# Kernel optimization log

Hardware: AMD Instinct MI355X
Metric: run time of the kernel (lower is better)

The kernel has to match this reference:

```python
import jax, jax.numpy as jnp
import numpy as np

EPS = 1e-5
B, D_ENT, D_REL = 1024, 400, 400
OUT, KW = 32, 9
N_ENT = 50000


def _bn(x, g, b, axes):
    # batch-norm with batch statistics (training-mode math), eps=1e-5
    mu = jnp.mean(x, axis=axes, keepdims=True)
    var = jnp.var(x, axis=axes, keepdims=True)
    return (x - mu) * jax.lax.rsqrt(var + EPS) * g + b


def setup_inputs() -> dict:
    key = jax.random.key(0)
    ks = jax.random.split(key, 6)
    return {
        "e1_emb": jax.random.normal(ks[0], (B, D_ENT), jnp.float32),
        "rel_emb": jax.random.normal(ks[1], (B, D_REL), jnp.float32),
        "all_ent_w": jax.random.normal(ks[2], (N_ENT, D_ENT), jnp.float32),
        "fc1_w": jax.random.normal(ks[3], (OUT * KW, D_REL), jnp.float32) * 0.05,
        "fc1_b": jnp.zeros((OUT * KW,), jnp.float32),
        "fc_w": jax.random.normal(ks[4], (D_ENT, (D_ENT - KW + 1) * OUT), jnp.float32) * 0.02,
        "fc_b": jnp.zeros((D_ENT,), jnp.float32),
        "bn0_g": jnp.ones((1,), jnp.float32),
        "bn0_b": jnp.zeros((1,), jnp.float32),
        "bn1_g": jnp.ones((OUT,), jnp.float32),
        "bn1_b": jnp.zeros((OUT,), jnp.float32),
        "bn2_g": jnp.ones((D_ENT,), jnp.float32),
        "bn2_b": jnp.zeros((D_ENT,), jnp.float32),
    }


def reference(e1_emb, rel_emb, all_ent_w, fc1_w, fc1_b, fc_w, fc_b,
              bn0_g, bn0_b, bn1_g, bn1_b, bn2_g, bn2_b):
    d = e1_emb.shape[1]
    L = d - KW + 1  # conv output width (kernel_h=1, in_channels=1)

    # bn0: BatchNorm2d(1) over view [B,1,1,d] -> stats over all elements
    x = _bn(e1_emb, bn0_g, bn0_b, axes=(0, 1))  # [B, d]

    # hypernetwork: relation -> per-sample conv kernels [B, OUT, KW]
    k = (rel_emb @ fc1_w.T + fc1_b).reshape(-1, OUT, KW)

    # per-sample 1x9 conv (groups=B) as windows + batched contraction
    # xw[b, l, w] = x[b, l + w]
    xw = jnp.stack([x[:, w:w + L] for w in range(KW)], axis=-1)  # [B, L, KW]
    conv = jnp.einsum('blw,bow->bol', xw, k)  # [B, OUT, L]

    # bn1: BatchNorm2d(OUT), per-channel stats over (batch, width)
    h = _bn(conv, bn1_g[None, :, None], bn1_b[None, :, None], axes=(0, 2))

    # flatten channel-major (matches torch .view(B, -1) on [B, OUT, 1, L])
    h = h.reshape(h.shape[0], OUT * L)
    h = h @ fc_w.T + fc_b  # [B, d]

    # bn2: BatchNorm1d(d), per-feature stats over batch
    h = jax.nn.relu(_bn(h, bn2_g, bn2_b, axes=(0,)))

    return h @ all_ent_w.T  # [B, N_ENT]
```

## Files before the change

kernel.cpp:

```cpp
#include <hip/hip_runtime.h>
#include <stdint.h>

typedef unsigned short u16;
typedef short bf16x8 __attribute__((ext_vector_type(8)));
typedef float f32x4 __attribute__((ext_vector_type(4)));
typedef u16 u16x4 __attribute__((ext_vector_type(4)));
typedef u16 u16x8 __attribute__((ext_vector_type(8)));

#define B_SZ   1024
#define D_IN   400
#define L_OUT  392
#define OC     32
#define KW     9
#define K_FC   12544
#define N_ENT  50000
#define NPAD_ENT 50048
#define KPAD_H 448
#define NPAD_FC 512
#define SPLIT_FC 14

__device__ __forceinline__ u16 f2bf(float f) {
  uint32_t u = __builtin_bit_cast(uint32_t, f);
  u += 0x7FFFu + ((u >> 16) & 1u);
  return (u16)(u >> 16);
}
__device__ __forceinline__ float bf2f(u16 v) {
  uint32_t u = ((uint32_t)v) << 16;
  return __builtin_bit_cast(float, u);
}

__device__ __forceinline__ void gload_lds16(const u16* g, u16* l) {
  __builtin_amdgcn_global_load_lds(
      (const __attribute__((address_space(1))) unsigned int*)g,
      (__attribute__((address_space(3))) unsigned int*)l, 16, 0, 0);
}

__device__ __forceinline__ void block_reduce2(float& s1, float& s2, float* sm) {
  for (int d = 32; d; d >>= 1) { s1 += __shfl_down(s1, d); s2 += __shfl_down(s2, d); }
  int wave = threadIdx.x >> 6, lane = threadIdx.x & 63;
  if (lane == 0) { sm[wave * 2] = s1; sm[wave * 2 + 1] = s2; }
  __syncthreads();
  if (threadIdx.x == 0) {
    s1 = sm[0] + sm[2] + sm[4] + sm[6];
    s2 = sm[1] + sm[3] + sm[5] + sm[7];
  }
}

__global__ __launch_bounds__(256) void red0(const float* __restrict__ e1, float* __restrict__ part0) {
  int t = threadIdx.x;
  int idx = blockIdx.x * 256 + t;
  float s1 = 0.f, s2 = 0.f;
  for (int i = idx; i < B_SZ * D_IN; i += 256 * 256) { float v = e1[i]; s1 += v; s2 += v * v; }
  __shared__ float sm[8];
  block_reduce2(s1, s2, sm);
  if (t == 0) { part0[blockIdx.x * 2] = s1; part0[blockIdx.x * 2 + 1] = s2; }
}

__global__ __launch_bounds__(256) void comb0(const float* __restrict__ part0,
                                             const float* __restrict__ g0,
                                             const float* __restrict__ b0,
                                             float* __restrict__ stats) {
  int t = threadIdx.x;
  float s1 = part0[t * 2], s2 = part0[t * 2 + 1];
  __shared__ float sm[8];
  block_reduce2(s1, s2, sm);
  if (t == 0) {
    const float N = (float)(B_SZ * D_IN);
    float mu = s1 / N, var = s2 / N - mu * mu;
    float a = g0[0] * rsqrtf(var + 1e-5f);
    stats[0] = a;
    stats[1] = b0[0] - mu * a;
  }
}

__global__ __launch_bounds__(256) void fc1_gemm(const float* __restrict__ rel,
                                                const float* __restrict__ W,
                                                const float* __restrict__ bias,
                                                float* __restrict__ outk) {
  __shared__ __align__(16) float As[16 * 68];
  __shared__ __align__(16) float Bs[16 * 68];
  int mt = blockIdx.x, nt = blockIdx.y;
  int t = threadIdx.x;
  int tx = t & 15, ty = t >> 4;
  int lr = t >> 2, lk = (t & 3) * 4;
  float acc[4][4] = {};
  for (int k0 = 0; k0 < 400; k0 += 16) {
    __syncthreads();
    float4 av = *(const float4*)(rel + (size_t)(mt * 64 + lr) * 400 + k0 + lk);
    int brow = nt * 64 + lr;
    float4 bv = {0.f, 0.f, 0.f, 0.f};
    if (brow < 288) bv = *(const float4*)(W + (size_t)brow * 400 + k0 + lk);
    As[(lk + 0) * 68 + lr] = av.x; As[(lk + 1) * 68 + lr] = av.y;
    As[(lk + 2) * 68 + lr] = av.z; As[(lk + 3) * 68 + lr] = av.w;
    Bs[(lk + 0) * 68 + lr] = bv.x; Bs[(lk + 1) * 68 + lr] = bv.y;
    Bs[(lk + 2) * 68 + lr] = bv.z; Bs[(lk + 3) * 68 + lr] = bv.w;
    __syncthreads();
#pragma unroll
    for (int k = 0; k < 16; ++k) {
      float4 a = *(const float4*)(As + k * 68 + ty * 4);
      float4 b = *(const float4*)(Bs + k * 68 + tx * 4);
      float aa[4] = {a.x, a.y, a.z, a.w}, bb[4] = {b.x, b.y, b.z, b.w};
#pragma unroll
      for (int i = 0; i < 4; ++i)
#pragma unroll
        for (int j = 0; j < 4; ++j) acc[i][j] += aa[i] * bb[j];
    }
  }
#pragma unroll
  for (int i = 0; i < 4; ++i) {
    int row = mt * 64 + ty * 4 + i;
#pragma unroll
    for (int j = 0; j < 4; ++j) {
      int col = nt * 64 + tx * 4 + j;
      if (col < 288) outk[(size_t)row * 288 + col] = acc[i][j] + bias[col];
    }
  }
}

__global__ __launch_bounds__(256) void conv_kernel(const float* __restrict__ e1,
                                                   const float* __restrict__ stats,
                                                   const float* __restrict__ kbuf,
                                                   u16* __restrict__ convA,
                                                   float* __restrict__ partial1) {
  int b = blockIdx.x, t = threadIdx.x;
  __shared__ __align__(16) float xs[D_IN];
  __shared__ float ks[OC * KW];
  float a0 = stats[0], b0c = stats[1];
  for (int i = t; i < D_IN; i += 256) xs[i] = e1[(size_t)b * D_IN + i] * a0 + b0c;
  for (int i = t; i < OC * KW; i += 256) ks[i] = kbuf[(size_t)b * (OC * KW) + i];
  __syncthreads();
  int o = t >> 3, sub = t & 7;
  float kw[KW];
#pragma unroll
  for (int w = 0; w < KW; ++w) kw[w] = ks[o * KW + w];
  float s1 = 0.f, s2 = 0.f;
  u16* orow = convA + (size_t)b * K_FC + o * L_OUT;
#pragma unroll
  for (int it = 0; it < 13; ++it) {
    int l = sub * 4 + it * 32;
    if (l < L_OUT) {
      float4 x0 = *(const float4*)(xs + l);
      float4 x1 = *(const float4*)(xs + l + 4);
      float4 x2 = *(const float4*)(xs + l + 8);
      float xv[12] = {x0.x, x0.y, x0.z, x0.w, x1.x, x1.y, x1.z, x1.w, x2.x, x2.y, x2.z, x2.w};
      u16x4 st;
#pragma unroll
      for (int j = 0; j < 4; ++j) {
        float c = 0.f;
#pragma unroll
        for (int w = 0; w < KW; ++w) c += xv[j + w] * kw[w];
        s1 += c; s2 += c * c;
        st[j] = f2bf(c);
      }
      *(u16x4*)(orow + l) = st;
    }
  }
  s1 += __shfl_down(s1, 4); s2 += __shfl_down(s2, 4);
  s1 += __shfl_down(s1, 2); s2 += __shfl_down(s2, 2);
  s1 += __shfl_down(s1, 1); s2 += __shfl_down(s2, 1);
  if (sub == 0) {
    partial1[b * 64 + o] = s1;
    partial1[b * 64 + 32 + o] = s2;
  }
}

__global__ __launch_bounds__(256) void comb1(const float* __restrict__ partial1,
                                             const float* __restrict__ g1,
                                             float* __restrict__ alphaK) {
  __shared__ float red[256];
  __shared__ float ab[32];
  int t = threadIdx.x;
  int s = t & 63, q = t >> 6;
  float acc = 0.f;
  for (int b = q * 256; b < q * 256 + 256; ++b) acc += partial1[b * 64 + s];
  red[t] = acc;
  __syncthreads();
  if (t < 64) red[t] = red[t] + red[t + 64] + red[t + 128] + red[t + 192];
  __syncthreads();
  if (t < 32) {
    const float N = (float)(B_SZ * L_OUT);
    float S1 = red[t], S2 = red[t + 32];
    float mu = S1 / N, var = S2 / N - mu * mu;
    ab[t] = g1[t] * rsqrtf(var + 1e-5f);
  }
  __syncthreads();
  for (int i = t; i < K_FC; i += 256) {
    int o = i / L_OUT;
    alphaK[i] = ab[o];
  }
}

__global__ __launch_bounds__(256) void cvt_fcw(const float* __restrict__ src,
                                               const float* __restrict__ alphaK,
                                               u16* __restrict__ dst) {
  int gid = blockIdx.x * 256 + threadIdx.x;
  int row = gid / 1568, c = gid - row * 1568;
  int k = c * 8;
  u16x8 o = {};
  if (row < 400) {
    float4 f0 = *(const float4*)(src + (size_t)row * K_FC + k);
    float4 f1 = *(const float4*)(src + (size_t)row * K_FC + k + 4);
    float4 a0 = *(const float4*)(alphaK + k);
    float4 a1 = *(const float4*)(alphaK + k + 4);
    o[0] = f2bf(f0.x * a0.x); o[1] = f2bf(f0.y * a0.y);
    o[2] = f2bf(f0.z * a0.z); o[3] = f2bf(f0.w * a0.w);
    o[4] = f2bf(f1.x * a1.x); o[5] = f2bf(f1.y * a1.y);
    o[6] = f2bf(f1.z * a1.z); o[7] = f2bf(f1.w * a1.w);
  }
  *(u16x8*)(dst + (size_t)row * K_FC + k) = o;
}

__global__ __launch_bounds__(256) void cvt_ent(const float* __restrict__ src, u16* __restrict__ dst) {
  int gid = blockIdx.x * 256 + threadIdx.x;
  int row = gid / 56, c = gid - row * 56;
  int k = c * 8;
  u16x8 o = {};
  if (row < N_ENT && k < D_IN) {
    float4 f0 = *(const float4*)(src + (size_t)row * D_IN + k);
    float4 f1 = *(const float4*)(src + (size_t)row * D_IN + k + 4);
    o[0] = f2bf(f0.x); o[1] = f2bf(f0.y); o[2] = f2bf(f0.z); o[3] = f2bf(f0.w);
    o[4] = f2bf(f1.x); o[5] = f2bf(f1.y); o[6] = f2bf(f1.z); o[7] = f2bf(f1.w);
  }
  *(u16x8*)(dst + (size_t)row * KPAD_H + k) = o;
}

__global__ __launch_bounds__(256) void bn2_kernel(const float* __restrict__ part2,
                                                  const float* __restrict__ g2,
                                                  const float* __restrict__ b2,
                                                  u16* __restrict__ hfin) {
  int j0 = blockIdx.x * 16;
  int t = threadIdx.x;
  int tj = t & 15, tb = t >> 4;
  int j = j0 + tj;
  float v[64];
  float s1 = 0.f, s2 = 0.f;
#pragma unroll 2
  for (int i = 0; i < 64; ++i) {
    int b = tb + i * 16;
    float acc = 0.f;
#pragma unroll
    for (int s = 0; s < SPLIT_FC; ++s)
      acc += part2[((size_t)s * B_SZ + b) * NPAD_FC + j];
    v[i] = acc; s1 += acc; s2 += acc * acc;
  }
  __shared__ float sm1[16][17], sm2[16][17];
  sm1[tb][tj] = s1; sm2[tb][tj] = s2;
  __syncthreads();
  __shared__ float albe[2][16];
  if (t < 16) {
    float S1 = 0.f, S2 = 0.f;
#pragma unroll
    for (int r = 0; r < 16; ++r) { S1 += sm1[r][t]; S2 += sm2[r][t]; }
    int jf = j0 + t;
    float al = 0.f, be = 0.f;
    if (jf < D_IN) {
      float mu = S1 / 1024.f, var = S2 / 1024.f - mu * mu;
      al = g2[jf] * rsqrtf(var + 1e-5f);
      be = b2[jf] - mu * al;
    }
    albe[0][t] = al; albe[1][t] = be;
  }
  __syncthreads();
  float al = albe[0][tj], be = albe[1][tj];
#pragma unroll 2
  for (int i = 0; i < 64; ++i) {
    int b = tb + i * 16;
    hfin[(size_t)b * KPAD_H + j] = f2bf(fmaxf(v[i] * al + be, 0.f));
  }
}

__global__ __launch_bounds__(256) void gemm_bt(const u16* __restrict__ A,
                                               const u16* __restrict__ Bm,
                                               float* __restrict__ C,
                                               int Kpad, int mtiles, int ntiles,
                                               int ksteps_total, int ksteps_chunk,
                                               long ldc, int ncols_valid, long csplit_stride,
                                               int xcd_swz) {
  __shared__ __align__(16) u16 As[128 * 64];
  __shared__ __align__(16) u16 Bs[128 * 64];
  int bid = blockIdx.x;
  int mt, nt, sp;
  if (xcd_swz) {
    int r = bid & 7, g = bid >> 3;
    mt = g & 7;
    nt = (g >> 3) * 8 + r;
    sp = 0;
    if (nt >= ntiles) return;
  } else {
    mt = bid % mtiles;
    nt = (bid / mtiles) % ntiles;
    sp = bid / (mtiles * ntiles);
  }
  int kbeg = sp * ksteps_chunk;
  int kend = kbeg + ksteps_chunk;
  if (kend > ksteps_total) kend = ksteps_total;

  int tid = threadIdx.x;
  int wave = tid >> 6, lane = tid & 63;
  int quad = lane >> 4, m16 = lane & 15;
  int rbase = (wave >> 1) * 64, cbase = (wave & 1) * 64;

  const u16* Arow0 = A + (size_t)mt * 128 * Kpad;
  const u16* Brow0 = Bm + (size_t)nt * 128 * Kpad;

  f32x4 acc[4][4] = {};

  for (int kt = kbeg; kt < kend; ++kt) {
    int k0 = kt * 64;
    __syncthreads();
#pragma unroll
    for (int p = 0; p < 4; ++p) {
      int slin = p * 256 + tid;
      int row = slin >> 3;
      int gch = (slin & 7) ^ (row & 7);
      u16* la = As + ((p * 256 + (wave << 6)) << 3);
      u16* lb = Bs + ((p * 256 + (wave << 6)) << 3);
      gload_lds16(Arow0 + (size_t)row * Kpad + k0 + gch * 8, la);
      gload_lds16(Brow0 + (size_t)row * Kpad + k0 + gch * 8, lb);
    }
    __syncthreads();
#pragma unroll
    for (int s = 0; s < 2; ++s) {
      bf16x8 af[4], bfr[4];
#pragma unroll
      for (int i = 0; i < 4; ++i) {
        int ar = rbase + i * 16 + m16;
        af[i] = *(const bf16x8*)(As + ar * 64 + (((s * 4 + quad) ^ (ar & 7)) << 3));
        int bc = cbase + i * 16 + m16;
        bfr[i] = *(const bf16x8*)(Bs + bc * 64 + (((s * 4 + quad) ^ (bc & 7)) << 3));
      }
#pragma unroll
      for (int i = 0; i < 4; ++i)
#pragma unroll
        for (int j = 0; j < 4; ++j)
          acc[i][j] = __builtin_amdgcn_mfma_f32_16x16x32_bf16(af[i], bfr[j], acc[i][j], 0, 0, 0);
    }
  }

  float* Cb = C + (size_t)sp * csplit_stride;
#pragma unroll
  for (int i = 0; i < 4; ++i) {
#pragma unroll
    for (int j = 0; j < 4; ++j) {
      int col = nt * 128 + cbase + j * 16 + m16;
      if (col < ncols_valid) {
        int row0 = mt * 128 + rbase + i * 16 + quad * 4;
#pragma unroll
        for (int r = 0; r < 4; ++r)
          Cb[(size_t)(row0 + r) * ldc + col] = acc[i][j][r];
      }
    }
  }
}

extern "C" void kernel_launch(void* const* d_in, const int* in_sizes, int n_in,
                              void* d_out, int out_size, void* d_ws, size_t ws_size,
                              hipStream_t stream) {
  const float* e1   = (const float*)d_in[0];
  const float* rel  = (const float*)d_in[1];
  const float* entw = (const float*)d_in[2];
  const float* fc1w = (const float*)d_in[3];
  const float* fc1b = (const float*)d_in[4];
  const float* fcw  = (const float*)d_in[5];
  const float* bn0g = (const float*)d_in[7];
  const float* bn0b = (const float*)d_in[8];
  const float* bn1g = (const float*)d_in[9];
  const float* bn2g = (const float*)d_in[11];
  const float* bn2b = (const float*)d_in[12];
  float* out = (float*)d_out;

  char* ws = (char*)d_ws;
  size_t off = 0;
  auto alloc = [&](size_t bytes) -> void* {
    off = (off + 255) & ~(size_t)255;
    void* p = ws + off;
    off += bytes;
    return p;
  };
  float* stats    = (float*)alloc(16 * 4);
  float* part0    = (float*)alloc(512 * 4);
  float* kbuf     = (float*)alloc((size_t)B_SZ * 288 * 4);
  float* partial1 = (float*)alloc((size_t)B_SZ * 64 * 4);
  float* alphaK   = (float*)alloc((size_t)K_FC * 4);
  u16*   convA    = (u16*)alloc((size_t)B_SZ * K_FC * 2);
  u16*   fcwb     = (u16*)alloc((size_t)NPAD_FC * K_FC * 2);
  float* part2    = (float*)alloc((size_t)SPLIT_FC * B_SZ * NPAD_FC * 4);
  u16*   hfin     = (u16*)alloc((size_t)B_SZ * KPAD_H * 2);
  u16*   entb     = (u16*)alloc((size_t)NPAD_ENT * KPAD_H * 2);

  red0<<<256, 256, 0, stream>>>(e1, part0);
  comb0<<<1, 256, 0, stream>>>(part0, bn0g, bn0b, stats);
  fc1_gemm<<<dim3(16, 5), 256, 0, stream>>>(rel, fc1w, fc1b, kbuf);
  conv_kernel<<<B_SZ, 256, 0, stream>>>(e1, stats, kbuf, convA, partial1);
  comb1<<<1, 256, 0, stream>>>(partial1, bn1g, alphaK);
  cvt_fcw<<<3136, 256, 0, stream>>>(fcw, alphaK, fcwb);
  gemm_bt<<<8 * 4 * SPLIT_FC, 256, 0, stream>>>(convA, fcwb, part2, K_FC, 8, 4, 196, 14,
                                                (long)NPAD_FC, NPAD_FC, (long)B_SZ * NPAD_FC, 0);
  bn2_kernel<<<KPAD_H / 16, 256, 0, stream>>>(part2, bn2g, bn2b, hfin);
  cvt_ent<<<10948, 256, 0, stream>>>(entw, entb);
  gemm_bt<<<8 * 392, 256, 0, stream>>>(hfin, entb, out, KPAD_H, 8, 391, 7, 7,
                                       (long)N_ENT, N_ENT, 0, 1);
}
```

Measured before the change: 555.4 us.

## Fuse fp32-to-bf16 weight conversion into GEMM loads and parallelize bn2

Drops the separate cvt_fcw and cvt_ent passes. Both GEMMs now read the fp32 weights directly, scaling and converting them to bf16 in registers before writing to LDS, which removes a full write and re-read of the converted weight buffers. The single-pass bn2 kernel, which ran on only 28 blocks, is split into stats, combine and apply kernels spread over 448 blocks. In exchange, the B-operand loads become synchronous register loads instead of async global-to-LDS loads. Each entity tile's weights are also converted again by all 8 M-tiles, which repeats conversion ALU work and doubles fp32 reads per tile.

After: 587.0 us. +5.7%, slower.

```diff
diff --git a/kernel.cpp b/kernel.cpp
--- a/kernel.cpp
+++ b/kernel.cpp
@@ -14,7 +14,6 @@
 #define KW     9
 #define K_FC   12544
 #define N_ENT  50000
-#define NPAD_ENT 50048
 #define KPAD_H 448
 #define NPAD_FC 512
 #define SPLIT_FC 14
@@ -23,10 +22,6 @@
   uint32_t u = __builtin_bit_cast(uint32_t, f);
   u += 0x7FFFu + ((u >> 16) & 1u);
   return (u16)(u >> 16);
-}
-__device__ __forceinline__ float bf2f(u16 v) {
-  uint32_t u = ((uint32_t)v) << 16;
-  return __builtin_bit_cast(float, u);
 }
 
 __device__ __forceinline__ void gload_lds16(const u16* g, u16* l) {
@@ -190,118 +185,22 @@
   }
 }
 
-__global__ __launch_bounds__(256) void cvt_fcw(const float* __restrict__ src,
+__global__ __launch_bounds__(256) void gemm_fc(const u16* __restrict__ A,
+                                               const float* __restrict__ Bw,
                                                const float* __restrict__ alphaK,
-                                               u16* __restrict__ dst) {
-  int gid = blockIdx.x * 256 + threadIdx.x;
-  int row = gid / 1568, c = gid - row * 1568;
-  int k = c * 8;
-  u16x8 o = {};
-  if (row < 400) {
-    float4 f0 = *(const float4*)(src + (size_t)row * K_FC + k);
-    float4 f1 = *(const float4*)(src + (size_t)row * K_FC + k + 4);
-    float4 a0 = *(const float4*)(alphaK + k);
-    float4 a1 = *(const float4*)(alphaK + k + 4);
-    o[0] = f2bf(f0.x * a0.x); o[1] = f2bf(f0.y * a0.y);
-    o[2] = f2bf(f0.z * a0.z); o[3] = f2bf(f0.w * a0.w);
-    o[4] = f2bf(f1.x * a1.x); o[5] = f2bf(f1.y * a1.y);
-    o[6] = f2bf(f1.z * a1.z); o[7] = f2bf(f1.w * a1.w);
-  }
-  *(u16x8*)(dst + (size_t)row * K_FC + k) = o;
-}
-
-__global__ __launch_bounds__(256) void cvt_ent(const float* __restrict__ src, u16* __restrict__ dst) {
-  int gid = blockIdx.x * 256 + threadIdx.x;
-  int row = gid / 56, c = gid - row * 56;
-  int k = c * 8;
-  u16x8 o = {};
-  if (row < N_ENT && k < D_IN) {
-    float4 f0 = *(const float4*)(src + (size_t)row * D_IN + k);
-    float4 f1 = *(const float4*)(src + (size_t)row * D_IN + k + 4);
-    o[0] = f2bf(f0.x); o[1] = f2bf(f0.y); o[2] = f2bf(f0.z); o[3] = f2bf(f0.w);
-    o[4] = f2bf(f1.x); o[5] = f2bf(f1.y); o[6] = f2bf(f1.z); o[7] = f2bf(f1.w);
-  }
-  *(u16x8*)(dst + (size_t)row * KPAD_H + k) = o;
-}
-
-__global__ __launch_bounds__(256) void bn2_kernel(const float* __restrict__ part2,
-                                                  const float* __restrict__ g2,
-                                                  const float* __restrict__ b2,
-                                                  u16* __restrict__ hfin) {
-  int j0 = blockIdx.x * 16;
-  int t = threadIdx.x;
-  int tj = t & 15, tb = t >> 4;
-  int j = j0 + tj;
-  float v[64];
-  float s1 = 0.f, s2 = 0.f;
-#pragma unroll 2
-  for (int i = 0; i < 64; ++i) {
-    int b = tb + i * 16;
-    float acc = 0.f;
-#pragma unroll
-    for (int s = 0; s < SPLIT_FC; ++s)
-      acc += part2[((size_t)s * B_SZ + b) * NPAD_FC + j];
-    v[i] = acc; s1 += acc; s2 += acc * acc;
-  }
-  __shared__ float sm1[16][17], sm2[16][17];
-  sm1[tb][tj] = s1; sm2[tb][tj] = s2;
-  __syncthreads();
-  __shared__ float albe[2][16];
-  if (t < 16) {
-    float S1 = 0.f, S2 = 0.f;
-#pragma unroll
-    for (int r = 0; r < 16; ++r) { S1 += sm1[r][t]; S2 += sm2[r][t]; }
-    int jf = j0 + t;
-    float al = 0.f, be = 0.f;
-    if (jf < D_IN) {
-      float mu = S1 / 1024.f, var = S2 / 1024.f - mu * mu;
-      al = g2[jf] * rsqrtf(var + 1e-5f);
-      be = b2[jf] - mu * al;
-    }
-    albe[0][t] = al; albe[1][t] = be;
-  }
-  __syncthreads();
-  float al = albe[0][tj], be = albe[1][tj];
-#pragma unroll 2
-  for (int i = 0; i < 64; ++i) {
-    int b = tb + i * 16;
-    hfin[(size_t)b * KPAD_H + j] = f2bf(fmaxf(v[i] * al + be, 0.f));
-  }
-}
-
-__global__ __launch_bounds__(256) void gemm_bt(const u16* __restrict__ A,
-                                               const u16* __restrict__ Bm,
-                                               float* __restrict__ C,
-                                               int Kpad, int mtiles, int ntiles,
-                                               int ksteps_total, int ksteps_chunk,
-                                               long ldc, int ncols_valid, long csplit_stride,
-                                               int xcd_swz) {
+                                               float* __restrict__ C) {
   __shared__ __align__(16) u16 As[128 * 64];
   __shared__ __align__(16) u16 Bs[128 * 64];
   int bid = blockIdx.x;
-  int mt, nt, sp;
-  if (xcd_swz) {
-    int r = bid & 7, g = bid >> 3;
-    mt = g & 7;
-    nt = (g >> 3) * 8 + r;
-    sp = 0;
-    if (nt >= ntiles) return;
-  } else {
-    mt = bid % mtiles;
-    nt = (bid / mtiles) % ntiles;
-    sp = bid / (mtiles * ntiles);
-  }
-  int kbeg = sp * ksteps_chunk;
-  int kend = kbeg + ksteps_chunk;
-  if (kend > ksteps_total) kend = ksteps_total;
+  int mt = bid & 7, nt = (bid >> 3) & 3, sp = bid >> 5;
+  int kbeg = sp * (196 / SPLIT_FC), kend = kbeg + (196 / SPLIT_FC);
 
   int tid = threadIdx.x;
   int wave = tid >> 6, lane = tid & 63;
   int quad = lane >> 4, m16 = lane & 15;
   int rbase = (wave >> 1) * 64, cbase = (wave & 1) * 64;
 
-  const u16* Arow0 = A + (size_t)mt * 128 * Kpad;
-  const u16* Brow0 = Bm + (size_t)nt * 128 * Kpad;
+  const u16* Arow0 = A + (size_t)mt * 128 * K_FC;
 
   f32x4 acc[4][4] = {};
 
@@ -313,10 +212,28 @@
       int slin = p * 256 + tid;
       int row = slin >> 3;
       int gch = (slin & 7) ^ (row & 7);
-      u16* la = As + ((p * 256 + (wave << 6)) << 3);
-      u16* lb = Bs + ((p * 256 + (wave << 6)) << 3);
-      gload_lds16(Arow0 + (size_t)row * Kpad + k0 + gch * 8, la);
-      gload_lds16(Brow0 + (size_t)row * Kpad + k0 + gch * 8, lb);
+      gload_lds16(Arow0 + (size_t)row * K_FC + k0 + gch * 8,
+                  As + ((p * 256 + (wave << 6)) << 3));
+    }
+#pragma unroll
+    for (int p = 0; p < 4; ++p) {
+      int slin = p * 256 + tid;
+      int row = slin >> 3;
+      int gch = (slin & 7) ^ (row & 7);
+      int gr = nt * 128 + row;
+      int k = k0 + gch * 8;
+      u16x8 bv = {};
+      if (gr < D_IN) {
+        float4 f0 = *(const float4*)(Bw + (size_t)gr * K_FC + k);
+        float4 f1 = *(const float4*)(Bw + (size_t)gr * K_FC + k + 4);
+        float4 a0 = *(const float4*)(alphaK + k);
+        float4 a1 = *(const float4*)(alphaK + k + 4);
+        bv[0] = f2bf(f0.x * a0.x); bv[1] = f2bf(f0.y * a0.y);
+        bv[2] = f2bf(f0.z * a0.z); bv[3] = f2bf(f0.w * a0.w);
+        bv[4] = f2bf(f1.x * a1.x); bv[5] = f2bf(f1.y * a1.y);
+        bv[6] = f2bf(f1.z * a1.z); bv[7] = f2bf(f1.w * a1.w);
+      }
+      *(u16x8*)(Bs + ((size_t)slin << 3)) = bv;
     }
     __syncthreads();
 #pragma unroll
@@ -337,17 +254,165 @@
     }
   }
 
-  float* Cb = C + (size_t)sp * csplit_stride;
+  float* Cb = C + (size_t)sp * B_SZ * NPAD_FC;
 #pragma unroll
   for (int i = 0; i < 4; ++i) {
 #pragma unroll
     for (int j = 0; j < 4; ++j) {
       int col = nt * 128 + cbase + j * 16 + m16;
-      if (col < ncols_valid) {
+      int row0 = mt * 128 + rbase + i * 16 + quad * 4;
+#pragma unroll
+      for (int r = 0; r < 4; ++r)
+        Cb[(size_t)(row0 + r) * NPAD_FC + col] = acc[i][j][r];
+    }
+  }
+}
+
+__global__ __launch_bounds__(256) void bn2_stats(const float* __restrict__ part2,
+                                                 float* __restrict__ pstat) {
+  int jg = blockIdx.x % 28, bc = blockIdx.x / 28;
+  int t = threadIdx.x;
+  int tj = t & 15, tb = t >> 4;
+  int j = jg * 16 + tj;
+  float s1 = 0.f, s2 = 0.f;
+#pragma unroll
+  for (int i = 0; i < 4; ++i) {
+    int b = bc * 64 + tb + i * 16;
+    float acc = 0.f;
+#pragma unroll
+    for (int s = 0; s < SPLIT_FC; ++s)
+      acc += part2[((size_t)s * B_SZ + b) * NPAD_FC + j];
+    s1 += acc; s2 += acc * acc;
+  }
+  __shared__ float sm1[16][17], sm2[16][17];
+  sm1[tb][tj] = s1; sm2[tb][tj] = s2;
+  __syncthreads();
+  if (t < 16) {
+    float S1 = 0.f, S2 = 0.f;
+#pragma unroll
+    for (int r = 0; r < 16; ++r) { S1 += sm1[r][t]; S2 += sm2[r][t]; }
+    pstat[blockIdx.x * 32 + t] = S1;
+    pstat[blockIdx.x * 32 + 16 + t] = S2;
+  }
+}
+
+__global__ __launch_bounds__(448) void bn2_comb(const float* __restrict__ pstat,
+                                                const float* __restrict__ g2,
+                                                const float* __restrict__ b2,
+                                                float* __restrict__ albe) {
+  int j = threadIdx.x;
+  int jg = j >> 4, tj = j & 15;
+  float S1 = 0.f, S2 = 0.f;
+#pragma unroll
+  for (int bc = 0; bc < 16; ++bc) {
+    S1 += pstat[(jg + 28 * bc) * 32 + tj];
+    S2 += pstat[(jg + 28 * bc) * 32 + 16 + tj];
+  }
+  float al = 0.f, be = 0.f;
+  if (j < D_IN) {
+    float mu = S1 / 1024.f, var = S2 / 1024.f - mu * mu;
+    al = g2[j] * rsqrtf(var + 1e-5f);
+    be = b2[j] - mu * al;
+  }
+  albe[j] = al;
+  albe[KPAD_H + j] = be;
+}
+
+__global__ __launch_bounds__(256) void bn2_apply(const float* __restrict__ part2,
+                                                 const float* __restrict__ albe,
+                                                 u16* __restrict__ hfin) {
+  int jg = blockIdx.x % 28, bc = blockIdx.x / 28;
+  int t = threadIdx.x;
+  int tj = t & 15, tb = t >> 4;
+  int j = jg * 16 + tj;
+  float al = albe[j], be = albe[KPAD_H + j];
+#pragma unroll
+  for (int i = 0; i < 4; ++i) {
+    int b = bc * 64 + tb + i * 16;
+    float acc = 0.f;
+#pragma unroll
+    for (int s = 0; s < SPLIT_FC; ++s)
+      acc += part2[((size_t)s * B_SZ + b) * NPAD_FC + j];
+    hfin[(size_t)b * KPAD_H + j] = f2bf(fmaxf(acc * al + be, 0.f));
+  }
+}
+
+__global__ __launch_bounds__(256) void gemm_ent(const u16* __restrict__ A,
+                                                const float* __restrict__ Bw,
+                                                float* __restrict__ C) {
+  __shared__ __align__(16) u16 As[128 * 64];
+  __shared__ __align__(16) u16 Bs[128 * 64];
+  int bid = blockIdx.x;
+  int r = bid & 7, g = bid >> 3;
+  int mt = g & 7;
+  int nt = (g >> 3) * 8 + r;
+  if (nt >= 391) return;
+
+  int tid = threadIdx.x;
+  int wave = tid >> 6, lane = tid & 63;
+  int quad = lane >> 4, m16 = lane & 15;
+  int rbase = (wave >> 1) * 64, cbase = (wave & 1) * 64;
+
+  const u16* Arow0 = A + (size_t)mt * 128 * KPAD_H;
+
+  f32x4 acc[4][4] = {};
+
+  for (int kt = 0; kt < 7; ++kt) {
+    int k0 = kt * 64;
+    __syncthreads();
+#pragma unroll
+    for (int p = 0; p < 4; ++p) {
+      int slin = p * 256 + tid;
+      int row = slin >> 3;
+      int gch = (slin & 7) ^ (row & 7);
+      gload_lds16(Arow0 + (size_t)row * KPAD_H + k0 + gch * 8,
+                  As + ((p * 256 + (wave << 6)) << 3));
+    }
+#pragma unroll
+    for (int p = 0; p < 4; ++p) {
+      int slin = p * 256 + tid;
+      int row = slin >> 3;
+      int gch = (slin & 7) ^ (row & 7);
+      int gr = nt * 128 + row;
+      int k = k0 + gch * 8;
+      u16x8 bv = {};
+      if (gr < N_ENT && k < D_IN) {
+        float4 f0 = *(const float4*)(Bw + (size_t)gr * D_IN + k);
+        float4 f1 = *(const float4*)(Bw + (size_t)gr * D_IN + k + 4);
+        bv[0] = f2bf(f0.x); bv[1] = f2bf(f0.y); bv[2] = f2bf(f0.z); bv[3] = f2bf(f0.w);
+        bv[4] = f2bf(f1.x); bv[5] = f2bf(f1.y); bv[6] = f2bf(f1.z); bv[7] = f2bf(f1.w);
+      }
+      *(u16x8*)(Bs + ((size_t)slin << 3)) = bv;
+    }
+    __syncthreads();
+#pragma unroll
+    for (int s = 0; s < 2; ++s) {
+      bf16x8 af[4], bfr[4];
+#pragma unroll
+      for (int i = 0; i < 4; ++i) {
+        int ar = rbase + i * 16 + m16;
+        af[i] = *(const bf16x8*)(As + ar * 64 + (((s * 4 + quad) ^ (ar & 7)) << 3));
+        int bc = cbase + i * 16 + m16;
+        bfr[i] = *(const bf16x8*)(Bs + bc * 64 + (((s * 4 + quad) ^ (bc & 7)) << 3));
+      }
+#pragma unroll
+      for (int i = 0; i < 4; ++i)
+#pragma unroll
+        for (int j = 0; j < 4; ++j)
+          acc[i][j] = __builtin_amdgcn_mfma_f32_16x16x32_bf16(af[i], bfr[j], acc[i][j], 0, 0, 0);
+    }
+  }
+
+#pragma unroll
+  for (int i = 0; i < 4; ++i) {
+#pragma unroll
+    for (int j = 0; j < 4; ++j) {
+      int col = nt * 128 + cbase + j * 16 + m16;
+      if (col < N_ENT) {
         int row0 = mt * 128 + rbase + i * 16 + quad * 4;
 #pragma unroll
-        for (int r = 0; r < 4; ++r)
-          Cb[(size_t)(row0 + r) * ldc + col] = acc[i][j][r];
+        for (int r2 = 0; r2 < 4; ++r2)
+          C[(size_t)(row0 + r2) * N_ENT + col] = acc[i][j][r2];
       }
     }
   }
@@ -383,21 +448,19 @@
   float* partial1 = (float*)alloc((size_t)B_SZ * 64 * 4);
   float* alphaK   = (float*)alloc((size_t)K_FC * 4);
   u16*   convA    = (u16*)alloc((size_t)B_SZ * K_FC * 2);
-  u16*   fcwb     = (u16*)alloc((size_t)NPAD_FC * K_FC * 2);
   float* part2    = (float*)alloc((size_t)SPLIT_FC * B_SZ * NPAD_FC * 4);
+  float* pstat    = (float*)alloc((size_t)448 * 32 * 4);
+  float* albe     = (float*)alloc((size_t)2 * KPAD_H * 4);
   u16*   hfin     = (u16*)alloc((size_t)B_SZ * KPAD_H * 2);
-  u16*   entb     = (u16*)alloc((size_t)NPAD_ENT * KPAD_H * 2);
 
   red0<<<256, 256, 0, stream>>>(e1, part0);
   comb0<<<1, 256, 0, stream>>>(part0, bn0g, bn0b, stats);
   fc1_gemm<<<dim3(16, 5), 256, 0, stream>>>(rel, fc1w, fc1b, kbuf);
   conv_kernel<<<B_SZ, 256, 0, stream>>>(e1, stats, kbuf, convA, partial1);
   comb1<<<1, 256, 0, stream>>>(partial1, bn1g, alphaK);
-  cvt_fcw<<<3136, 256, 0, stream>>>(fcw, alphaK, fcwb);
-  gemm_bt<<<8 * 4 * SPLIT_FC, 256, 0, stream>>>(convA, fcwb, part2, K_FC, 8, 4, 196, 14,
-                                                (long)NPAD_FC, NPAD_FC, (long)B_SZ * NPAD_FC, 0);
-  bn2_kernel<<<KPAD_H / 16, 256, 0, stream>>>(part2, bn2g, bn2b, hfin);
-  cvt_ent<<<10948, 256, 0, stream>>>(entw, entb);
-  gemm_bt<<<8 * 392, 256, 0, stream>>>(hfin, entb, out, KPAD_H, 8, 391, 7, 7,
-                                       (long)N_ENT, N_ENT, 0, 1);
-}
+  gemm_fc<<<8 * 4 * SPLIT_FC, 256, 0, stream>>>(convA, fcw, alphaK, part2);
+  bn2_stats<<<28 * 16, 256, 0, stream>>>(part2, pstat);
+  bn2_comb<<<1, 448, 0, stream>>>(pstat, bn2g, bn2b, albe);
+  bn2_apply<<<28 * 16, 256, 0, stream>>>(part2, albe, hfin);
+  gemm_ent<<<8 * 392, 256, 0, stream>>>(hfin, entw, out);
+}
```
